# Kernel tuning notes

Hardware: AMD Instinct MI355X
Metric: run time of the kernel (lower is better)

The kernel has to match this reference:

```python
import jax, jax.numpy as jnp
import numpy as np

B, T, N, D = 16, 48, 256, 64
K_HEADS = 8


def setup_inputs() -> dict:
    key = jax.random.key(0)
    ks = jax.random.split(key, 12)
    return {
        "query": jax.random.normal(ks[0], (B, T, N, D), jnp.float32),
        "key": jax.random.normal(ks[1], (B, T, N, D), jnp.float32),
        "value": jax.random.normal(ks[2], (B, T, N, D), jnp.float32),
        "key_w": jax.random.normal(ks[3], (B, T, D, D), jnp.float32) * 0.05,
        "key_b": jax.random.normal(ks[4], (B, T, D), jnp.float32) * 0.05,
        "value_w": jax.random.normal(ks[5], (B, T, D, D), jnp.float32) * 0.05,
        "value_b": jax.random.normal(ks[6], (B, T, D), jnp.float32) * 0.05,
        "proj1_w": jax.random.normal(ks[7], (D, D), jnp.float32) * 0.05,
        "proj1_b": jax.random.normal(ks[8], (D,), jnp.float32) * 0.05,
        "proj2_w": jax.random.normal(ks[9], (D, D), jnp.float32) * 0.05,
        "proj2_b": jax.random.normal(ks[10], (D,), jnp.float32) * 0.05,
        "rate": jnp.full((1,), 0.8, jnp.float32),
    }


def reference(query, key, value, key_w, key_b, value_w, value_b,
              proj1_w, proj1_b, proj2_w, proj2_b, rate):
    b, t, n, d = query.shape
    hs = d // K_HEADS
    # per-(batch,time) projections (LinearCustom)
    k = jnp.einsum('btnd,btde->btne', key, key_w) + key_b[:, :, None, :]
    v = jnp.einsum('btnd,btde->btne', value, value_w) + value_b[:, :, None, :]
    # split heads along channel dim (matches torch.split on dim -1)
    qh = query.reshape(b, t, n, K_HEADS, hs)
    kh = k.reshape(b, t, n, K_HEADS, hs)
    vh = v.reshape(b, t, n, K_HEADS, hs)
    # scores: [b, h, n, q, k]
    scores = jnp.einsum('bqnhd,bknhd->bhnqk', qh, kh) / jnp.sqrt(jnp.asarray(hs, query.dtype))
    # time decay: b_time_decays[..., i, j] = (T-1-i) + 1 = T - i (depends on query pos only)
    dec = (t - jnp.arange(t, dtype=scores.dtype))[:, None]  # [T, 1], broadcasts over key axis
    s = jax.nn.sigmoid(scores)
    denom = 1.0 + jax.nn.sigmoid(s * jax.nn.sigmoid(rate) * dec)
    att = jax.nn.softmax(jnp.tanh(s / denom), axis=-1)
    x = jnp.einsum('bhnqk,bknhd->bqnhd', att, vh).reshape(b, t, n, d)
    x = jnp.tanh(x @ proj1_w.T + proj1_b)
    return x @ proj2_w.T + proj2_b
```

## Files before the change

### kernel.cpp

```cpp
#include <hip/hip_runtime.h>


#define B_ 16
#define T_ 48
#define N_ 256
#define D_ 64
#define H_ 8
#define HS_ 8

__device__ __forceinline__ float rcpf(float x) { return __builtin_amdgcn_rcpf(x); }
__device__ __forceinline__ float ex2(float x) { return __builtin_amdgcn_exp2f(x); }

#define LOG2E 1.4426950408889634f

__global__ __launch_bounds__(256) void proj_kv_kernel(
    const float* __restrict__ key, const float* __restrict__ key_w, const float* __restrict__ key_b,
    const float* __restrict__ value, const float* __restrict__ value_w, const float* __restrict__ value_b,
    float* __restrict__ k_out, float* __restrict__ v_out)
{
    const int bt = blockIdx.x;
    const int which = blockIdx.y;
    const float* __restrict__ in = (which ? value : key) + (size_t)bt * N_ * D_;
    const float* __restrict__ w  = (which ? value_w : key_w) + (size_t)bt * D_ * D_;
    const float* __restrict__ bb = (which ? value_b : key_b) + (size_t)bt * D_;
    float* __restrict__ out = (which ? v_out : k_out) + (size_t)bt * N_ * D_;

    __shared__ float Wl[D_][D_];
    __shared__ float Xl[128][68];
    __shared__ float Bl[D_];

    const int tid = threadIdx.x;
    #pragma unroll
    for (int i = tid; i < D_ * D_; i += 256) Wl[i >> 6][i & 63] = w[i];
    if (tid < D_) Bl[tid] = bb[tid];

    const int cg = tid & 7;
    const int rg = tid >> 3;

    for (int n0 = 0; n0 < N_; n0 += 128) {
        __syncthreads();
        #pragma unroll
        for (int i = tid; i < 128 * D_ / 4; i += 256) {
            const int e = i * 4;
            *(float4*)&Xl[e >> 6][e & 63] = *(const float4*)&in[(size_t)n0 * D_ + e];
        }
        __syncthreads();

        float acc[4][8];
        #pragma unroll
        for (int j = 0; j < 4; ++j)
            #pragma unroll
            for (int i = 0; i < 8; ++i) acc[j][i] = Bl[cg * 8 + i];

        #pragma unroll 8
        for (int d = 0; d < D_; ++d) {
            const float4 w0 = *(const float4*)&Wl[d][cg * 8];
            const float4 w1 = *(const float4*)&Wl[d][cg * 8 + 4];
            #pragma unroll
            for (int j = 0; j < 4; ++j) {
                const float a = Xl[rg + 32 * j][d];
                acc[j][0] += a * w0.x; acc[j][1] += a * w0.y;
                acc[j][2] += a * w0.z; acc[j][3] += a * w0.w;
                acc[j][4] += a * w1.x; acc[j][5] += a * w1.y;
                acc[j][6] += a * w1.z; acc[j][7] += a * w1.w;
            }
        }

        #pragma unroll
        for (int j = 0; j < 4; ++j) {
            const size_t row = (size_t)(n0 + rg + 32 * j);
            *(float4*)&out[row * D_ + cg * 8]     = make_float4(acc[j][0], acc[j][1], acc[j][2], acc[j][3]);
            *(float4*)&out[row * D_ + cg * 8 + 4] = make_float4(acc[j][4], acc[j][5], acc[j][6], acc[j][7]);
        }
    }
}

__global__ __launch_bounds__(192) void attn_kernel(
    const float* __restrict__ query, float* __restrict__ k_xatt, const float* __restrict__ v_in,
    const float* __restrict__ rate)
{
    const int b  = blockIdx.x >> 7;
    const int n0 = (blockIdx.x & 127) * 2;

    __shared__ float K[2][T_][D_];
    __shared__ float V[2][T_][D_];

    const int tid = threadIdx.x;
    #pragma unroll
    for (int i = tid; i < T_ * 16; i += 192) {
        const int t = i >> 4, d4 = (i & 15) * 4;
        const size_t g0 = ((size_t)(b * T_ + t) * N_ + n0) * D_ + d4;
        *(float4*)&K[0][t][d4] = *(const float4*)&k_xatt[g0];
        *(float4*)&V[0][t][d4] = *(const float4*)&v_in[g0];
        *(float4*)&K[1][t][d4] = *(const float4*)&k_xatt[g0 + D_];
        *(float4*)&V[1][t][d4] = *(const float4*)&v_in[g0 + D_];
    }
    const float rsig = rcpf(1.0f + ex2(-rate[0] * LOG2E));

    const int nl  = tid / 96;
    const int r96 = tid % 96;
    const int qg  = r96 >> 3;
    const int h   = r96 & 7;
    const int n   = n0 + nl;

    const float C1 = 0.35355339059327373f * LOG2E;
    float4 qa[4], qb[4];
    float rdn[4];
    #pragma unroll
    for (int j = 0; j < 4; ++j) {
        const int q = qg + 12 * j;
        const size_t g = ((size_t)(b * T_ + q) * N_ + n) * D_ + h * 8;
        const float4 a = *(const float4*)&query[g];
        const float4 c = *(const float4*)&query[g + 4];
        qa[j] = make_float4(-C1 * a.x, -C1 * a.y, -C1 * a.z, -C1 * a.w);
        qb[j] = make_float4(-C1 * c.x, -C1 * c.y, -C1 * c.z, -C1 * c.w);
        rdn[j] = -rsig * (float)(T_ - q) * LOG2E;
    }
    __syncthreads();

    float4 acc0[4], acc1[4];
    float ssum[4];
    #pragma unroll
    for (int j = 0; j < 4; ++j) {
        acc0[j] = make_float4(0.f, 0.f, 0.f, 0.f);
        acc1[j] = make_float4(0.f, 0.f, 0.f, 0.f);
        ssum[j] = 0.f;
    }

    #pragma unroll 2
    for (int tk = 0; tk < T_; ++tk) {
        const float4 ka = *(const float4*)&K[nl][tk][h * 8];
        const float4 kb = *(const float4*)&K[nl][tk][h * 8 + 4];
        const float4 va = *(const float4*)&V[nl][tk][h * 8];
        const float4 vb = *(const float4*)&V[nl][tk][h * 8 + 4];
        #pragma unroll
        for (int j = 0; j < 4; ++j) {
            const float dn = qa[j].x * ka.x + qa[j].y * ka.y + qa[j].z * ka.z + qa[j].w * ka.w
                           + qb[j].x * kb.x + qb[j].y * kb.y + qb[j].z * kb.z + qb[j].w * kb.w;
            const float s   = rcpf(1.0f + ex2(dn));
            const float s2  = rcpf(1.0f + ex2(s * rdn[j]));
            const float arg = s * rcpf(1.0f + s2);
            const float th  = 1.0f - 2.0f * rcpf(ex2(arg * (2.0f * LOG2E)) + 1.0f);
            const float e   = ex2(th * LOG2E);
            ssum[j] += e;
            acc0[j].x += e * va.x; acc0[j].y += e * va.y; acc0[j].z += e * va.z; acc0[j].w += e * va.w;
            acc1[j].x += e * vb.x; acc1[j].y += e * vb.y; acc1[j].z += e * vb.z; acc1[j].w += e * vb.w;
        }
    }

    #pragma unroll
    for (int j = 0; j < 4; ++j) {
        const float inv = rcpf(ssum[j]);
        const int q = qg + 12 * j;
        const size_t g = ((size_t)(b * T_ + q) * N_ + n) * D_ + h * 8;
        *(float4*)&k_xatt[g]     = make_float4(acc0[j].x * inv, acc0[j].y * inv, acc0[j].z * inv, acc0[j].w * inv);
        *(float4*)&k_xatt[g + 4] = make_float4(acc1[j].x * inv, acc1[j].y * inv, acc1[j].z * inv, acc1[j].w * inv);
    }
}

__global__ __launch_bounds__(128) void out_proj_kernel(
    const float* __restrict__ xatt,
    const float* __restrict__ p1w, const float* __restrict__ p1b,
    const float* __restrict__ p2w, const float* __restrict__ p2b,
    float* __restrict__ out)
{
    __shared__ float X[128][68];
    __shared__ float W1t[D_][68];
    __shared__ float W2t[D_][68];
    __shared__ float B1[D_], B2[D_];

    const int tid = threadIdx.x;
    const size_t m0 = (size_t)blockIdx.x * 128;

    #pragma unroll
    for (int i = tid; i < D_ * D_; i += 128) {
        const int c = i >> 6, d = i & 63;
        W1t[d][c] = p1w[i];
        W2t[d][c] = p2w[i];
    }
    #pragma unroll
    for (int i = tid; i < 128 * 16; i += 128) {
        const int row = i >> 4, d4 = (i & 15) * 4;
        *(float4*)&X[row][d4] = *(const float4*)&xatt[(m0 + row) * D_ + d4];
    }
    if (tid < D_) { B1[tid] = p1b[tid]; B2[tid] = p2b[tid]; }
    __syncthreads();

    const int cg = tid & 7;
    const int rg = tid >> 3;

    float x1[8][8];
    {
        float acc[8][8];
        #pragma unroll
        for (int j = 0; j < 8; ++j)
            #pragma unroll
            for (int i = 0; i < 8; ++i) acc[j][i] = B1[cg * 8 + i];

        #pragma unroll 4
        for (int d0 = 0; d0 < D_; d0 += 4) {
            float4 w0[4], w1[4];
            #pragma unroll
            for (int dd = 0; dd < 4; ++dd) {
                w0[dd] = *(const float4*)&W1t[d0 + dd][cg * 8];
                w1[dd] = *(const float4*)&W1t[d0 + dd][cg * 8 + 4];
            }
            #pragma unroll
            for (int j = 0; j < 8; ++j) {
                const float4 xv = *(const float4*)&X[rg + 16 * j][d0];
                acc[j][0] += xv.x * w0[0].x + xv.y * w0[1].x + xv.z * w0[2].x + xv.w * w0[3].x;
                acc[j][1] += xv.x * w0[0].y + xv.y * w0[1].y + xv.z * w0[2].y + xv.w * w0[3].y;
                acc[j][2] += xv.x * w0[0].z + xv.y * w0[1].z + xv.z * w0[2].z + xv.w * w0[3].z;
                acc[j][3] += xv.x * w0[0].w + xv.y * w0[1].w + xv.z * w0[2].w + xv.w * w0[3].w;
                acc[j][4] += xv.x * w1[0].x + xv.y * w1[1].x + xv.z * w1[2].x + xv.w * w1[3].x;
                acc[j][5] += xv.x * w1[0].y + xv.y * w1[1].y + xv.z * w1[2].y + xv.w * w1[3].y;
                acc[j][6] += xv.x * w1[0].z + xv.y * w1[1].z + xv.z * w1[2].z + xv.w * w1[3].z;
                acc[j][7] += xv.x * w1[0].w + xv.y * w1[1].w + xv.z * w1[2].w + xv.w * w1[3].w;
            }
        }
        #pragma unroll
        for (int j = 0; j < 8; ++j)
            #pragma unroll
            for (int i = 0; i < 8; ++i)
                x1[j][i] = 1.0f - 2.0f * rcpf(ex2(acc[j][i] * (2.0f * LOG2E)) + 1.0f);
    }
    __syncthreads();
    #pragma unroll
    for (int j = 0; j < 8; ++j) {
        *(float4*)&X[rg + 16 * j][cg * 8]     = make_float4(x1[j][0], x1[j][1], x1[j][2], x1[j][3]);
        *(float4*)&X[rg + 16 * j][cg * 8 + 4] = make_float4(x1[j][4], x1[j][5], x1[j][6], x1[j][7]);
    }
    __syncthreads();

    {
        float acc[8][8];
        #pragma unroll
        for (int j = 0; j < 8; ++j)
            #pragma unroll
            for (int i = 0; i < 8; ++i) acc[j][i] = B2[cg * 8 + i];

        #pragma unroll 4
        for (int d0 = 0; d0 < D_; d0 += 4) {
            float4 w0[4], w1[4];
            #pragma unroll
            for (int dd = 0; dd < 4; ++dd) {
                w0[dd] = *(const float4*)&W2t[d0 + dd][cg * 8];
                w1[dd] = *(const float4*)&W2t[d0 + dd][cg * 8 + 4];
            }
            #pragma unroll
            for (int j = 0; j < 8; ++j) {
                const float4 xv = *(const float4*)&X[rg + 16 * j][d0];
                acc[j][0] += xv.x * w0[0].x + xv.y * w0[1].x + xv.z * w0[2].x + xv.w * w0[3].x;
                acc[j][1] += xv.x * w0[0].y + xv.y * w0[1].y + xv.z * w0[2].y + xv.w * w0[3].y;
                acc[j][2] += xv.x * w0[0].z + xv.y * w0[1].z + xv.z * w0[2].z + xv.w * w0[3].z;
                acc[j][3] += xv.x * w0[0].w + xv.y * w0[1].w + xv.z * w0[2].w + xv.w * w0[3].w;
                acc[j][4] += xv.x * w1[0].x + xv.y * w1[1].x + xv.z * w1[2].x + xv.w * w1[3].x;
                acc[j][5] += xv.x * w1[0].y + xv.y * w1[1].y + xv.z * w1[2].y + xv.w * w1[3].y;
                acc[j][6] += xv.x * w1[0].z + xv.y * w1[1].z + xv.z * w1[2].z + xv.w * w1[3].z;
                acc[j][7] += xv.x * w1[0].w + xv.y * w1[1].w + xv.z * w1[2].w + xv.w * w1[3].w;
            }
        }
        #pragma unroll
        for (int j = 0; j < 8; ++j) {
            const size_t og = (m0 + rg + 16 * j) * D_ + cg * 8;
            *(float4*)&out[og]     = make_float4(acc[j][0], acc[j][1], acc[j][2], acc[j][3]);
            *(float4*)&out[og + 4] = make_float4(acc[j][4], acc[j][5], acc[j][6], acc[j][7]);
        }
    }
}

extern "C" void kernel_launch(void* const* d_in, const int* in_sizes, int n_in,
                              void* d_out, int out_size, void* d_ws, size_t ws_size,
                              hipStream_t stream) {
    const float* query   = (const float*)d_in[0];
    const float* key     = (const float*)d_in[1];
    const float* value   = (const float*)d_in[2];
    const float* key_w   = (const float*)d_in[3];
    const float* key_b   = (const float*)d_in[4];
    const float* value_w = (const float*)d_in[5];
    const float* value_b = (const float*)d_in[6];
    const float* p1w     = (const float*)d_in[7];
    const float* p1b     = (const float*)d_in[8];
    const float* p2w     = (const float*)d_in[9];
    const float* p2b     = (const float*)d_in[10];
    const float* rate    = (const float*)d_in[11];
    float* out = (float*)d_out;

    float* kws = (float*)d_ws;
    float* vws = kws + (size_t)B_ * T_ * N_ * D_;

    dim3 gridA(B_ * T_, 2);
    proj_kv_kernel<<<gridA, 256, 0, stream>>>(key, key_w, key_b, value, value_w, value_b, kws, vws);
    attn_kernel<<<B_ * (N_ / 2), 192, 0, stream>>>(query, kws, vws, rate);
    out_proj_kernel<<<(B_ * T_ * N_) / 128, 128, 0, stream>>>(kws, p1w, p1b, p2w, p2b, out);
}
```

Before: 276.2 us.

## Rework attention thread mapping, rational tanh, and out-proj with pre-transposed weights

The attention kernel now runs 256 threads, each handling 3 queries instead of 4, and pads its shared K/V rows to reduce bank conflicts. The inner tanh is replaced by a rational approximation. The output projection moves weight transposition into a separate small kernel and restructures the two GEMMs: activations are transposed in LDS and the weights are read through scalar (readfirstlane) broadcast loads. The aim is to raise occupancy and cut LDS staging cost. The rational tanh is only accurate for small arguments, which holds here because the argument stays in [0,1). Placing the transposed weights in the V workspace after attention finishes is safe on the same stream.

Measured after the change: 241.6 us. -12.5%, faster.

```diff
diff --git a/kernel.cpp b/kernel.cpp
--- a/kernel.cpp
+++ b/kernel.cpp
@@ -5,12 +5,9 @@
 #define T_ 48
 #define N_ 256
 #define D_ 64
-#define H_ 8
-#define HS_ 8
 
 __device__ __forceinline__ float rcpf(float x) { return __builtin_amdgcn_rcpf(x); }
 __device__ __forceinline__ float ex2(float x) { return __builtin_amdgcn_exp2f(x); }
-
 #define LOG2E 1.4426950408889634f
 
 __global__ __launch_bounds__(256) void proj_kv_kernel(
@@ -75,19 +72,19 @@
     }
 }
 
-__global__ __launch_bounds__(192) void attn_kernel(
+__global__ __launch_bounds__(256) void attn_kernel(
     const float* __restrict__ query, float* __restrict__ k_xatt, const float* __restrict__ v_in,
     const float* __restrict__ rate)
 {
     const int b  = blockIdx.x >> 7;
     const int n0 = (blockIdx.x & 127) * 2;
 
-    __shared__ float K[2][T_][D_];
-    __shared__ float V[2][T_][D_];
+    __shared__ float K[2][T_][68];
+    __shared__ float V[2][T_][68];
 
     const int tid = threadIdx.x;
     #pragma unroll
-    for (int i = tid; i < T_ * 16; i += 192) {
+    for (int i = tid; i < T_ * 16; i += 256) {
         const int t = i >> 4, d4 = (i & 15) * 4;
         const size_t g0 = ((size_t)(b * T_ + t) * N_ + n0) * D_ + d4;
         *(float4*)&K[0][t][d4] = *(const float4*)&k_xatt[g0];
@@ -97,18 +94,18 @@
     }
     const float rsig = rcpf(1.0f + ex2(-rate[0] * LOG2E));
 
-    const int nl  = tid / 96;
-    const int r96 = tid % 96;
-    const int qg  = r96 >> 3;
-    const int h   = r96 & 7;
-    const int n   = n0 + nl;
+    const int nl = tid >> 7;
+    const int r  = tid & 127;
+    const int qg = r >> 3;
+    const int h  = r & 7;
+    const int n  = n0 + nl;
 
     const float C1 = 0.35355339059327373f * LOG2E;
-    float4 qa[4], qb[4];
-    float rdn[4];
-    #pragma unroll
-    for (int j = 0; j < 4; ++j) {
-        const int q = qg + 12 * j;
+    float4 qa[3], qb[3];
+    float rdn[3];
+    #pragma unroll
+    for (int j = 0; j < 3; ++j) {
+        const int q = qg + 16 * j;
         const size_t g = ((size_t)(b * T_ + q) * N_ + n) * D_ + h * 8;
         const float4 a = *(const float4*)&query[g];
         const float4 c = *(const float4*)&query[g + 4];
@@ -118,10 +115,10 @@
     }
     __syncthreads();
 
-    float4 acc0[4], acc1[4];
-    float ssum[4];
-    #pragma unroll
-    for (int j = 0; j < 4; ++j) {
+    float4 acc0[3], acc1[3];
+    float ssum[3];
+    #pragma unroll
+    for (int j = 0; j < 3; ++j) {
         acc0[j] = make_float4(0.f, 0.f, 0.f, 0.f);
         acc1[j] = make_float4(0.f, 0.f, 0.f, 0.f);
         ssum[j] = 0.f;
@@ -134,13 +131,14 @@
         const float4 va = *(const float4*)&V[nl][tk][h * 8];
         const float4 vb = *(const float4*)&V[nl][tk][h * 8 + 4];
         #pragma unroll
-        for (int j = 0; j < 4; ++j) {
+        for (int j = 0; j < 3; ++j) {
             const float dn = qa[j].x * ka.x + qa[j].y * ka.y + qa[j].z * ka.z + qa[j].w * ka.w
                            + qb[j].x * kb.x + qb[j].y * kb.y + qb[j].z * kb.z + qb[j].w * kb.w;
             const float s   = rcpf(1.0f + ex2(dn));
             const float s2  = rcpf(1.0f + ex2(s * rdn[j]));
             const float arg = s * rcpf(1.0f + s2);
-            const float th  = 1.0f - 2.0f * rcpf(ex2(arg * (2.0f * LOG2E)) + 1.0f);
+            const float x2  = arg * arg;
+            const float th  = arg * (15.0f + x2) * rcpf(15.0f + 6.0f * x2);
             const float e   = ex2(th * LOG2E);
             ssum[j] += e;
             acc0[j].x += e * va.x; acc0[j].y += e * va.y; acc0[j].z += e * va.z; acc0[j].w += e * va.w;
@@ -149,123 +147,103 @@
     }
 
     #pragma unroll
-    for (int j = 0; j < 4; ++j) {
+    for (int j = 0; j < 3; ++j) {
         const float inv = rcpf(ssum[j]);
-        const int q = qg + 12 * j;
+        const int q = qg + 16 * j;
         const size_t g = ((size_t)(b * T_ + q) * N_ + n) * D_ + h * 8;
         *(float4*)&k_xatt[g]     = make_float4(acc0[j].x * inv, acc0[j].y * inv, acc0[j].z * inv, acc0[j].w * inv);
         *(float4*)&k_xatt[g + 4] = make_float4(acc1[j].x * inv, acc1[j].y * inv, acc1[j].z * inv, acc1[j].w * inv);
     }
 }
 
-__global__ __launch_bounds__(128) void out_proj_kernel(
+__global__ __launch_bounds__(256) void wtrans_kernel(
+    const float* __restrict__ p1w, const float* __restrict__ p2w,
+    float* __restrict__ w1t, float* __restrict__ w2t)
+{
+    const int i = blockIdx.x * 256 + threadIdx.x;
+    if (i < D_ * D_) {
+        const int d = i >> 6, c = i & 63;
+        w1t[i] = p1w[c * 64 + d];
+        w2t[i] = p2w[c * 64 + d];
+    }
+}
+
+__global__ __launch_bounds__(256) void out_proj_kernel(
     const float* __restrict__ xatt,
-    const float* __restrict__ p1w, const float* __restrict__ p1b,
-    const float* __restrict__ p2w, const float* __restrict__ p2b,
+    const float* __restrict__ w1t, const float* __restrict__ p1b,
+    const float* __restrict__ w2t, const float* __restrict__ p2b,
     float* __restrict__ out)
 {
-    __shared__ float X[128][68];
-    __shared__ float W1t[D_][68];
-    __shared__ float W2t[D_][68];
-    __shared__ float B1[D_], B2[D_];
+    __shared__ float Xt[D_][132];
 
     const int tid = threadIdx.x;
     const size_t m0 = (size_t)blockIdx.x * 128;
 
     #pragma unroll
-    for (int i = tid; i < D_ * D_; i += 128) {
-        const int c = i >> 6, d = i & 63;
-        W1t[d][c] = p1w[i];
-        W2t[d][c] = p2w[i];
-    }
-    #pragma unroll
-    for (int i = tid; i < 128 * 16; i += 128) {
+    for (int i = tid; i < 128 * 16; i += 256) {
         const int row = i >> 4, d4 = (i & 15) * 4;
-        *(float4*)&X[row][d4] = *(const float4*)&xatt[(m0 + row) * D_ + d4];
-    }
-    if (tid < D_) { B1[tid] = p1b[tid]; B2[tid] = p2b[tid]; }
-    __syncthreads();
-
-    const int cg = tid & 7;
-    const int rg = tid >> 3;
-
-    float x1[8][8];
-    {
-        float acc[8][8];
-        #pragma unroll
-        for (int j = 0; j < 8; ++j)
-            #pragma unroll
-            for (int i = 0; i < 8; ++i) acc[j][i] = B1[cg * 8 + i];
-
-        #pragma unroll 4
-        for (int d0 = 0; d0 < D_; d0 += 4) {
-            float4 w0[4], w1[4];
-            #pragma unroll
-            for (int dd = 0; dd < 4; ++dd) {
-                w0[dd] = *(const float4*)&W1t[d0 + dd][cg * 8];
-                w1[dd] = *(const float4*)&W1t[d0 + dd][cg * 8 + 4];
-            }
-            #pragma unroll
-            for (int j = 0; j < 8; ++j) {
-                const float4 xv = *(const float4*)&X[rg + 16 * j][d0];
-                acc[j][0] += xv.x * w0[0].x + xv.y * w0[1].x + xv.z * w0[2].x + xv.w * w0[3].x;
-                acc[j][1] += xv.x * w0[0].y + xv.y * w0[1].y + xv.z * w0[2].y + xv.w * w0[3].y;
-                acc[j][2] += xv.x * w0[0].z + xv.y * w0[1].z + xv.z * w0[2].z + xv.w * w0[3].z;
-                acc[j][3] += xv.x * w0[0].w + xv.y * w0[1].w + xv.z * w0[2].w + xv.w * w0[3].w;
-                acc[j][4] += xv.x * w1[0].x + xv.y * w1[1].x + xv.z * w1[2].x + xv.w * w1[3].x;
-                acc[j][5] += xv.x * w1[0].y + xv.y * w1[1].y + xv.z * w1[2].y + xv.w * w1[3].y;
-                acc[j][6] += xv.x * w1[0].z + xv.y * w1[1].z + xv.z * w1[2].z + xv.w * w1[3].z;
-                acc[j][7] += xv.x * w1[0].w + xv.y * w1[1].w + xv.z * w1[2].w + xv.w * w1[3].w;
-            }
-        }
-        #pragma unroll
-        for (int j = 0; j < 8; ++j)
-            #pragma unroll
-            for (int i = 0; i < 8; ++i)
-                x1[j][i] = 1.0f - 2.0f * rcpf(ex2(acc[j][i] * (2.0f * LOG2E)) + 1.0f);
-    }
-    __syncthreads();
-    #pragma unroll
-    for (int j = 0; j < 8; ++j) {
-        *(float4*)&X[rg + 16 * j][cg * 8]     = make_float4(x1[j][0], x1[j][1], x1[j][2], x1[j][3]);
-        *(float4*)&X[rg + 16 * j][cg * 8 + 4] = make_float4(x1[j][4], x1[j][5], x1[j][6], x1[j][7]);
-    }
-    __syncthreads();
-
-    {
-        float acc[8][8];
-        #pragma unroll
-        for (int j = 0; j < 8; ++j)
-            #pragma unroll
-            for (int i = 0; i < 8; ++i) acc[j][i] = B2[cg * 8 + i];
-
-        #pragma unroll 4
-        for (int d0 = 0; d0 < D_; d0 += 4) {
-            float4 w0[4], w1[4];
-            #pragma unroll
-            for (int dd = 0; dd < 4; ++dd) {
-                w0[dd] = *(const float4*)&W2t[d0 + dd][cg * 8];
-                w1[dd] = *(const float4*)&W2t[d0 + dd][cg * 8 + 4];
-            }
-            #pragma unroll
-            for (int j = 0; j < 8; ++j) {
-                const float4 xv = *(const float4*)&X[rg + 16 * j][d0];
-                acc[j][0] += xv.x * w0[0].x + xv.y * w0[1].x + xv.z * w0[2].x + xv.w * w0[3].x;
-                acc[j][1] += xv.x * w0[0].y + xv.y * w0[1].y + xv.z * w0[2].y + xv.w * w0[3].y;
-                acc[j][2] += xv.x * w0[0].z + xv.y * w0[1].z + xv.z * w0[2].z + xv.w * w0[3].z;
-                acc[j][3] += xv.x * w0[0].w + xv.y * w0[1].w + xv.z * w0[2].w + xv.w * w0[3].w;
-                acc[j][4] += xv.x * w1[0].x + xv.y * w1[1].x + xv.z * w1[2].x + xv.w * w1[3].x;
-                acc[j][5] += xv.x * w1[0].y + xv.y * w1[1].y + xv.z * w1[2].y + xv.w * w1[3].y;
-                acc[j][6] += xv.x * w1[0].z + xv.y * w1[1].z + xv.z * w1[2].z + xv.w * w1[3].z;
-                acc[j][7] += xv.x * w1[0].w + xv.y * w1[1].w + xv.z * w1[2].w + xv.w * w1[3].w;
-            }
-        }
-        #pragma unroll
-        for (int j = 0; j < 8; ++j) {
-            const size_t og = (m0 + rg + 16 * j) * D_ + cg * 8;
-            *(float4*)&out[og]     = make_float4(acc[j][0], acc[j][1], acc[j][2], acc[j][3]);
-            *(float4*)&out[og + 4] = make_float4(acc[j][4], acc[j][5], acc[j][6], acc[j][7]);
-        }
+        const float4 xv = *(const float4*)&xatt[(m0 + row) * D_ + d4];
+        Xt[d4 + 0][row] = xv.x;
+        Xt[d4 + 1][row] = xv.y;
+        Xt[d4 + 2][row] = xv.z;
+        Xt[d4 + 3][row] = xv.w;
+    }
+    __syncthreads();
+
+    const int l  = tid & 63;
+    const int c0 = __builtin_amdgcn_readfirstlane((tid >> 6) * 16);
+
+    float a0[16], a1[16];
+    #pragma unroll
+    for (int c = 0; c < 16; ++c) {
+        const float bv = p1b[c0 + c];
+        a0[c] = bv; a1[c] = bv;
+    }
+    for (int d = 0; d < D_; ++d) {
+        const float x0 = Xt[d][l];
+        const float x1 = Xt[d][l + 64];
+        const float* wr = w1t + __builtin_amdgcn_readfirstlane(d * 64 + c0);
+        #pragma unroll
+        for (int c = 0; c < 16; ++c) {
+            const float wv = wr[c];
+            a0[c] += x0 * wv;
+            a1[c] += x1 * wv;
+        }
+    }
+    #pragma unroll
+    for (int c = 0; c < 16; ++c) {
+        a0[c] = 1.0f - 2.0f * rcpf(ex2(a0[c] * (2.0f * LOG2E)) + 1.0f);
+        a1[c] = 1.0f - 2.0f * rcpf(ex2(a1[c] * (2.0f * LOG2E)) + 1.0f);
+    }
+    __syncthreads();
+    #pragma unroll
+    for (int c = 0; c < 16; ++c) {
+        Xt[c0 + c][l]      = a0[c];
+        Xt[c0 + c][l + 64] = a1[c];
+    }
+    __syncthreads();
+
+    float o0[16], o1[16];
+    #pragma unroll
+    for (int c = 0; c < 16; ++c) {
+        const float bv = p2b[c0 + c];
+        o0[c] = bv; o1[c] = bv;
+    }
+    for (int d = 0; d < D_; ++d) {
+        const float x0 = Xt[d][l];
+        const float x1 = Xt[d][l + 64];
+        const float* wr = w2t + __builtin_amdgcn_readfirstlane(d * 64 + c0);
+        #pragma unroll
+        for (int c = 0; c < 16; ++c) {
+            const float wv = wr[c];
+            o0[c] += x0 * wv;
+            o1[c] += x1 * wv;
+        }
+    }
+    #pragma unroll
+    for (int k = 0; k < 4; ++k) {
+        *(float4*)&out[(m0 + l) * D_ + c0 + 4 * k]      = make_float4(o0[4*k], o0[4*k+1], o0[4*k+2], o0[4*k+3]);
+        *(float4*)&out[(m0 + l + 64) * D_ + c0 + 4 * k] = make_float4(o1[4*k], o1[4*k+1], o1[4*k+2], o1[4*k+3]);
     }
 }
 
@@ -288,9 +266,12 @@
 
     float* kws = (float*)d_ws;
     float* vws = kws + (size_t)B_ * T_ * N_ * D_;
+    float* w1t = vws;
+    float* w2t = vws + D_ * D_;
 
     dim3 gridA(B_ * T_, 2);
     proj_kv_kernel<<<gridA, 256, 0, stream>>>(key, key_w, key_b, value, value_w, value_b, kws, vws);
-    attn_kernel<<<B_ * (N_ / 2), 192, 0, stream>>>(query, kws, vws, rate);
-    out_proj_kernel<<<(B_ * T_ * N_) / 128, 128, 0, stream>>>(kws, p1w, p1b, p2w, p2b, out);
-}
+    attn_kernel<<<B_ * (N_ / 2), 256, 0, stream>>>(query, kws, vws, rate);
+    wtrans_kernel<<<16, 256, 0, stream>>>(p1w, p2w, w1t, w2t);
+    out_proj_kernel<<<(B_ * T_ * N_) / 128, 256, 0, stream>>>(kws, w1t, p1b, w2t, p2b, out);
+}
```
